# Kernel tuning notes

Hardware: AMD Instinct MI355X
Metric: run time of the kernel (lower is better)

The kernel has to match this reference:

```python
import jax, jax.numpy as jnp
import numpy as np

N = 50000
E = 800000
H = 128
K = 4
BN_EPS = 1e-5


def _cheb_norm(edge_index):
    # PyG ChebConv with normalization='sym', lambda_max=2.0:
    # L_hat = 2L/lambda_max - I = -D^{-1/2} A D^{-1/2}
    src, dst = edge_index[0], edge_index[1]
    deg = jax.ops.segment_sum(jnp.ones((E,), jnp.float32), src, num_segments=N)
    dinv = jnp.where(deg > 0, jax.lax.rsqrt(jnp.maximum(deg, 1.0)), 0.0)
    return -dinv[src] * dinv[dst]  # [E]


def _cheb_conv(x, src, dst, w, W, b):
    # Chebyshev recursion: Tx0=x, Tx1=L_hat x, Txk = 2 L_hat Tx_{k-1} - Tx_{k-2}
    def prop(h):
        return jax.ops.segment_sum(h[src] * w[:, None], dst, num_segments=N)
    Tx0 = x
    out = Tx0 @ W[0]
    Tx1 = prop(Tx0)
    out = out + Tx1 @ W[1]
    for k in range(2, W.shape[0]):
        Tx2 = 2.0 * prop(Tx1) - Tx0
        out = out + Tx2 @ W[k]
        Tx0, Tx1 = Tx1, Tx2
    return out + b


def _bn(h, gamma, beta):
    # BatchNorm1d, training mode: biased batch stats over nodes
    m = h.mean(axis=0)
    v = h.var(axis=0)
    return (h - m) * jax.lax.rsqrt(v + BN_EPS) * gamma + beta


def setup_inputs() -> dict:
    key = jax.random.key(0)
    ks = jax.random.split(key, 8)
    x = jax.random.normal(ks[0], (N, 3), jnp.float32)
    edge_index = jax.random.randint(ks[1], (2, E), 0, N, jnp.int64)
    s1 = 1.0 / np.sqrt(3)
    s2 = 1.0 / np.sqrt(H)
    d = {
        'x': x,
        'edge_index': edge_index,
        'W1': jax.random.normal(ks[2], (K, 3, H), jnp.float32) * s1,
        'b1': jnp.zeros((H,), jnp.float32),
        'W2': jax.random.normal(ks[3], (K, H, H), jnp.float32) * s2,
        'b2': jnp.zeros((H,), jnp.float32),
        'W3': jax.random.normal(ks[4], (K, H, H), jnp.float32) * s2,
        'b3': jnp.zeros((H,), jnp.float32),
        'W4': jax.random.normal(ks[5], (K, H, H), jnp.float32) * s2,
        'b4': jnp.zeros((H,), jnp.float32),
        'g1': jnp.ones((H,), jnp.float32), 'be1': jnp.zeros((H,), jnp.float32),
        'g2': jnp.ones((H,), jnp.float32), 'be2': jnp.zeros((H,), jnp.float32),
        'g3': jnp.ones((H,), jnp.float32), 'be3': jnp.zeros((H,), jnp.float32),
    }
    return d


def reference(x, edge_index, W1, b1, W2, b2, W3, b3, W4, b4, g1, be1, g2, be2, g3, be3):
    src, dst = edge_index[0], edge_index[1]
    w = _cheb_norm(edge_index)
    h = _bn(jax.nn.leaky_relu(_cheb_conv(x, src, dst, w, W1, b1)), g1, be1)
    h = _bn(jax.nn.leaky_relu(_cheb_conv(h, src, dst, w, W2, b2)), g2, be2)
    h = _bn(jax.nn.relu(_cheb_conv(h, src, dst, w, W3, b3)), g3, be3)
    h = _cheb_conv(h, src, dst, w, W4, b4)
    # F.normalize(p=2, dim=1)
    nrm = jnp.sqrt(jnp.sum(h * h, axis=1, keepdims=True))
    return h / jnp.maximum(nrm, 1e-12)
```

## Files before the change

kernel.cpp:

```cpp
#include <hip/hip_runtime.h>
#include <hip/hip_fp16.h>

#define NN 50000
#define NE 800000
#define HD 128
#define NSL 128
#define SLE (NE / NSL)
#define PW  12500

typedef __attribute__((ext_vector_type(8))) short short8;
typedef __attribute__((ext_vector_type(4))) float f32x4;
typedef __attribute__((ext_vector_type(4))) unsigned u32x4;

__device__ inline unsigned bf2pack(float lo, float hi) {
    unsigned a = __float_as_uint(lo); a = (a + 0x7fffu + ((a >> 16) & 1u)) >> 16;
    unsigned b = __float_as_uint(hi); b = (b + 0x7fffu + ((b >> 16) & 1u)) >> 16;
    return a | (b << 16);
}

__device__ inline float edgw(unsigned p) {
    return __half2float(__ushort_as_half((unsigned short)(p >> 16)));
}

__global__ __launch_bounds__(256) void k_hist(const int* __restrict__ ei,
                                              unsigned* __restrict__ phist) {
    __shared__ unsigned hist[PW];
    int b = blockIdx.x;
    int a = b >> 8;
    int s = (b & 255) >> 1;
    int c = b & 1;
    int tid = threadIdx.x;
    for (int i = tid; i < PW; i += 256) hist[i] = 0u;
    __syncthreads();
    const int* arr = ei + a * NE + s * SLE;
    int lo = c * 25000;
    for (int i = tid; i < SLE; i += 256) {
        int v = arr[i] - lo;
        if ((unsigned)v < 25000u)
            atomicAdd(&hist[v >> 1], 1u << ((v & 1) * 16));
    }
    __syncthreads();
    unsigned* dst = phist + (size_t)b * PW;
    for (int i = tid; i < PW; i += 256) dst[i] = hist[i];
}

__global__ __launch_bounds__(256) void k_hreduce(const unsigned* __restrict__ phist,
                                                 float* __restrict__ dinv,
                                                 int* __restrict__ cnt,
                                                 unsigned* __restrict__ pre) {
    int idx = blockIdx.x * 256 + threadIdx.x;
    if (idx >= 50000) return;
    int a = idx / 25000;
    int gw = idx % 25000;
    int c = gw / PW;
    int w = gw % PW;
    unsigned accLo = 0, accHi = 0;
    for (int s = 0; s < NSL; s++) {
        unsigned p = phist[(size_t)(((a * NSL + s) * 2 + c)) * PW + w];
        if (a == 1) pre[(size_t)s * 25000 + gw] = accLo | (accHi << 16);
        accLo += p & 0xffffu;
        accHi += p >> 16;
    }
    int b0 = c * 25000 + 2 * w;
    if (a == 0) {
        dinv[b0]     = accLo ? rsqrtf((float)accLo) : 0.0f;
        dinv[b0 + 1] = accHi ? rsqrtf((float)accHi) : 0.0f;
    } else {
        cnt[b0]     = (int)accLo;
        cnt[b0 + 1] = (int)accHi;
    }
}

__global__ __launch_bounds__(1024) void k_scan1(const int* __restrict__ cnt,
                                                int* __restrict__ rowptr,
                                                int* __restrict__ bsum) {
    __shared__ int s[1024];
    int tid = threadIdx.x;
    int gid = blockIdx.x * 1024 + tid;
    int v = (gid < NN) ? cnt[gid] : 0;
    s[tid] = v;
    __syncthreads();
    for (int off = 1; off < 1024; off <<= 1) {
        int t = 0;
        if (tid >= off) t = s[tid - off];
        __syncthreads();
        s[tid] += t;
        __syncthreads();
    }
    if (gid < NN) rowptr[gid] = s[tid] - v;
    if (tid == 1023) bsum[blockIdx.x] = s[1023];
}

__global__ void k_scan2(const int* __restrict__ bsum, int* __restrict__ boff,
                        int nb, int* __restrict__ rowptr) {
    if (threadIdx.x == 0 && blockIdx.x == 0) {
        int acc = 0;
        for (int i = 0; i < nb; i++) { boff[i] = acc; acc += bsum[i]; }
        rowptr[NN] = acc;
    }
}

__global__ void k_scan3(int* __restrict__ rowptr, const int* __restrict__ boff) {
    int i = blockIdx.x * 256 + threadIdx.x;
    if (i < NN) rowptr[i] += boff[i >> 10];
}

__global__ __launch_bounds__(256) void k_fill2(const int* __restrict__ ei,
                                               const float* __restrict__ dinv,
                                               const int* __restrict__ rowptr,
                                               const unsigned* __restrict__ pre,
                                               unsigned* __restrict__ edg) {
    __shared__ unsigned rank[PW];
    int b = blockIdx.x;
    int s = b >> 1;
    int c = b & 1;
    int tid = threadIdx.x;
    for (int i = tid; i < PW; i += 256) rank[i] = 0u;
    __syncthreads();
    int lo = c * 25000;
    const unsigned* preS = pre + (size_t)s * 25000 + c * PW;
    for (int i = tid; i < SLE; i += 256) {
        int e = s * SLE + i;
        int d = ei[NE + e];
        int v = d - lo;
        if ((unsigned)v < 25000u) {
            int src = ei[e];
            int w = v >> 1;
            int sh = (v & 1) * 16;
            unsigned r = atomicAdd(&rank[w], 1u << sh);
            r = (r >> sh) & 0xffffu;
            unsigned pw = (preS[w] >> sh) & 0xffffu;
            int pos = rowptr[d] + (int)pw + (int)r;
            unsigned short hw = __half_as_ushort(__float2half(-dinv[src] * dinv[d]));
            edg[pos] = (unsigned)src | ((unsigned)hw << 16);
        }
    }
}

__global__ void k_prop3(const float* __restrict__ h, const float* __restrict__ sub,
                        const int* __restrict__ rowptr, const unsigned* __restrict__ edg,
                        float* __restrict__ out) {
    int node = blockIdx.x * 256 + threadIdx.x;
    if (node >= NN) return;
    int e0 = rowptr[node], e1 = rowptr[node + 1];
    float a0 = 0.f, a1 = 0.f, a2 = 0.f;
    for (int e = e0; e < e1; e++) {
        unsigned p = edg[e];
        int s = p & 0xffffu;
        float v = edgw(p);
        a0 += v * h[s * 3 + 0];
        a1 += v * h[s * 3 + 1];
        a2 += v * h[s * 3 + 2];
    }
    if (sub) {
        a0 = 2.f * a0 - sub[node * 3 + 0];
        a1 = 2.f * a1 - sub[node * 3 + 1];
        a2 = 2.f * a2 - sub[node * 3 + 2];
    }
    out[node * 3 + 0] = a0;
    out[node * 3 + 1] = a1;
    out[node * 3 + 2] = a2;
}

#define ACC8(acc, u, v)                                               \
    acc[0] = fmaf(v, __uint_as_float(u[0] << 16), acc[0]);            \
    acc[1] = fmaf(v, __uint_as_float(u[0] & 0xffff0000u), acc[1]);    \
    acc[2] = fmaf(v, __uint_as_float(u[1] << 16), acc[2]);            \
    acc[3] = fmaf(v, __uint_as_float(u[1] & 0xffff0000u), acc[3]);    \
    acc[4] = fmaf(v, __uint_as_float(u[2] << 16), acc[4]);            \
    acc[5] = fmaf(v, __uint_as_float(u[2] & 0xffff0000u), acc[5]);    \
    acc[6] = fmaf(v, __uint_as_float(u[3] << 16), acc[6]);            \
    acc[7] = fmaf(v, __uint_as_float(u[3] & 0xffff0000u), acc[7]);

__global__ __launch_bounds__(256) void k_prop_pl(
        const unsigned short* __restrict__ h, const unsigned short* __restrict__ sub,
        const int* __restrict__ rowptr, const unsigned* __restrict__ edg,
        unsigned short* __restrict__ out) {
    int B = blockIdx.x;
    int xcd = B & 7;
    int c = xcd >> 1;
    int half = xcd & 1;
    int g = B >> 3;
    int n = (half * 392 + g) * 64 + (threadIdx.x >> 2);
    if (n >= NN) return;
    int lane4 = threadIdx.x & 3;
    int sl = lane4 * 8;
    int base = (threadIdx.x & 63) & ~3;
    const unsigned short* hp = h + (size_t)c * (NN * 32);
    int e0 = rowptr[n], e1 = rowptr[n + 1];
    float a[8] = {0, 0, 0, 0, 0, 0, 0, 0};
    float b[8] = {0, 0, 0, 0, 0, 0, 0, 0};
    int e = e0;
    for (; e + 8 <= e1; e += 8) {
        uint2 pp = *(const uint2*)(edg + e + lane4 * 2);
        unsigned q0 = __shfl(pp.x, base + 0, 64);
        unsigned q1 = __shfl(pp.y, base + 0, 64);
        unsigned q2 = __shfl(pp.x, base + 1, 64);
        unsigned q3 = __shfl(pp.y, base + 1, 64);
        unsigned q4 = __shfl(pp.x, base + 2, 64);
        unsigned q5 = __shfl(pp.y, base + 2, 64);
        unsigned q6 = __shfl(pp.x, base + 3, 64);
        unsigned q7 = __shfl(pp.y, base + 3, 64);
        u32x4 u0 = *(const u32x4*)(hp + (q0 & 0xffffu) * 32 + sl);
        u32x4 u1 = *(const u32x4*)(hp + (q1 & 0xffffu) * 32 + sl);
        u32x4 u2 = *(const u32x4*)(hp + (q2 & 0xffffu) * 32 + sl);
        u32x4 u3 = *(const u32x4*)(hp + (q3 & 0xffffu) * 32 + sl);
        u32x4 u4 = *(const u32x4*)(hp + (q4 & 0xffffu) * 32 + sl);
        u32x4 u5 = *(const u32x4*)(hp + (q5 & 0xffffu) * 32 + sl);
        u32x4 u6 = *(const u32x4*)(hp + (q6 & 0xffffu) * 32 + sl);
        u32x4 u7 = *(const u32x4*)(hp + (q7 & 0xffffu) * 32 + sl);
        float v0 = edgw(q0), v1 = edgw(q1), v2 = edgw(q2), v3 = edgw(q3);
        float v4 = edgw(q4), v5 = edgw(q5), v6 = edgw(q6), v7 = edgw(q7);
        ACC8(a, u0, v0)
        ACC8(b, u1, v1)
        ACC8(a, u2, v2)
        ACC8(b, u3, v3)
        ACC8(a, u4, v4)
        ACC8(b, u5, v5)
        ACC8(a, u6, v6)
        ACC8(b, u7, v7)
    }
    for (; e < e1; e++) {
        unsigned p = edg[e];
        u32x4 u = *(const u32x4*)(hp + (p & 0xffffu) * 32 + sl);
        float v = edgw(p);
        ACC8(a, u, v)
    }
    float r[8];
    #pragma unroll
    for (int q = 0; q < 8; q++) r[q] = a[q] + b[q];
    if (sub) {
        u32x4 su = __builtin_nontemporal_load(
            (const u32x4*)(sub + (size_t)c * (NN * 32) + n * 32 + sl));
        float s[8];
        s[0] = __uint_as_float(su[0] << 16); s[1] = __uint_as_float(su[0] & 0xffff0000u);
        s[2] = __uint_as_float(su[1] << 16); s[3] = __uint_as_float(su[1] & 0xffff0000u);
        s[4] = __uint_as_float(su[2] << 16); s[5] = __uint_as_float(su[2] & 0xffff0000u);
        s[6] = __uint_as_float(su[3] << 16); s[7] = __uint_as_float(su[3] & 0xffff0000u);
        #pragma unroll
        for (int q = 0; q < 8; q++) r[q] = 2.f * r[q] - s[q];
    }
    u32x4 o;
    o[0] = bf2pack(r[0], r[1]);
    o[1] = bf2pack(r[2], r[3]);
    o[2] = bf2pack(r[4], r[5]);
    o[3] = bf2pack(r[6], r[7]);
    __builtin_nontemporal_store(o, (u32x4*)(out + (size_t)c * (NN * 32) + n * 32 + sl));
}

__global__ void k_wconv_all(const float* __restrict__ W2, const float* __restrict__ W3,
                            const float* __restrict__ W4, unsigned short* __restrict__ Wb) {
    int gidx = blockIdx.x * 256 + threadIdx.x;
    int which = gidx >> 16;
    int idx = gidx & 65535;
    const float* W = which == 0 ? W2 : (which == 1 ? W3 : W4);
    int slot = idx >> 9;
    int lane = (idx >> 3) & 63;
    int j = idx & 7;
    int wg = slot >> 4;
    int t = slot & 15;
    int w = wg >> 1;
    int g = wg & 1;
    int k = t * 32 + (lane >> 4) * 8 + j;
    int col = w * 32 + g * 16 + (lane & 15);
    unsigned u = __float_as_uint(W[k * HD + col]);
    Wb[which * 65536 + idx] = (unsigned short)((u + 0x7fffu + ((u >> 16) & 1u)) >> 16);
}

__global__ __launch_bounds__(256) void k_gemmM(
        const unsigned short* __restrict__ A0, const unsigned short* __restrict__ A1,
        const unsigned short* __restrict__ A2, const unsigned short* __restrict__ A3,
        const unsigned short* __restrict__ Wb, const float* __restrict__ bias,
        float* __restrict__ outF, int act, float* __restrict__ gpart) {
    __shared__ unsigned short Asm[16 * 64 * 8];
    const int tid = threadIdx.x;
    const int w = tid >> 6;
    const int lane = tid & 63;
    const int l15 = lane & 15;
    const int quad = lane >> 4;

    short8 Bf[16][2];
    #pragma unroll
    for (int t = 0; t < 16; t++) {
        #pragma unroll
        for (int g = 0; g < 2; g++) {
            int slot = (w * 2 + g) * 16 + t;
            Bf[t][g] = *(const short8*)(Wb + slot * 512 + lane * 8);
        }
    }
    float bcol[2];
    bcol[0] = bias[w * 32 + l15];
    bcol[1] = bias[w * 32 + 16 + l15];

    const unsigned short* Ap[4] = {A0, A1, A2, A3};
    float bnP[2] = {0.f, 0.f}, bnQ[2] = {0.f, 0.f};

    for (int tile = blockIdx.x; tile < NN / 16; tile += gridDim.x) {
        int r0 = tile * 16;
        __syncthreads();
        #pragma unroll
        for (int i = 0; i < 4; i++) {
            int idx = i * 256 + tid;
            int s = idx >> 6;
            int ln = idx & 63;
            const unsigned short* src = Ap[s >> 2] + (size_t)(s & 3) * (NN * 32)
                                        + (r0 + (ln & 15)) * 32 + (ln >> 4) * 8;
            *(uint4*)&Asm[idx * 8] = *(const uint4*)src;
        }
        __syncthreads();
        f32x4 acc0 = {0.f, 0.f, 0.f, 0.f};
        f32x4 acc1 = {0.f, 0.f, 0.f, 0.f};
        #pragma unroll
        for (int s = 0; s < 16; s++) {
            short8 af = *(const short8*)&Asm[(s * 64 + lane) * 8];
            acc0 = __builtin_amdgcn_mfma_f32_16x16x32_bf16(af, Bf[s][0], acc0, 0, 0, 0);
            acc1 = __builtin_amdgcn_mfma_f32_16x16x32_bf16(af, Bf[s][1], acc1, 0, 0, 0);
        }
        #pragma unroll
        for (int reg = 0; reg < 4; reg++) {
            int row = r0 + quad * 4 + reg;
            float v0 = acc0[reg] + bcol[0];
            float v1 = acc1[reg] + bcol[1];
            if (act == 1) {
                v0 = v0 > 0.f ? v0 : 0.01f * v0;
                v1 = v1 > 0.f ? v1 : 0.01f * v1;
            } else if (act == 2) {
                v0 = v0 > 0.f ? v0 : 0.f;
                v1 = v1 > 0.f ? v1 : 0.f;
            }
            outF[row * HD + w * 32 + l15] = v0;
            outF[row * HD + w * 32 + 16 + l15] = v1;
            bnP[0] += v0; bnQ[0] += v0 * v0;
            bnP[1] += v1; bnQ[1] += v1 * v1;
        }
    }
    if (gpart) {
        #pragma unroll
        for (int g = 0; g < 2; g++) {
            float p = bnP[g], q = bnQ[g];
            p += __shfl_xor(p, 16); p += __shfl_xor(p, 32);
            q += __shfl_xor(q, 16); q += __shfl_xor(q, 32);
            if (quad == 0) {
                int col = w * 32 + g * 16 + l15;
                gpart[col * 512 + blockIdx.x] = p;
                gpart[(128 + col) * 512 + blockIdx.x] = q;
            }
        }
    }
}

__global__ __launch_bounds__(256) void k_gemm1(
        const float* __restrict__ T0, const float* __restrict__ T1,
        const float* __restrict__ T2, const float* __restrict__ T3,
        const float* __restrict__ W, const float* __restrict__ bias,
        float* __restrict__ out) {
    __shared__ float Ws[12 * 128];
    __shared__ float tx[2][12];
    int t = threadIdx.x;
    for (int i = t; i < 12 * 128; i += 256) Ws[i] = W[i];
    int idx = blockIdx.x * 256 + t;
    int node = idx >> 7;
    int f = idx & 127;
    int localn = t >> 7;
    const float* Ts[4] = {T0, T1, T2, T3};
    if (f < 12 && node < NN) {
        tx[localn][f] = Ts[f / 3][node * 3 + (f % 3)];
    }
    __syncthreads();
    if (node < NN) {
        float acc = bias[f];
        #pragma unroll
        for (int c = 0; c < 12; c++) acc = fmaf(tx[localn][c], Ws[c * 128 + f], acc);
        acc = acc > 0.f ? acc : 0.01f * acc;
        out[node * HD + f] = acc;
    }
}

__global__ __launch_bounds__(256) void k_bnstats2(const float* __restrict__ h,
                                                  float* __restrict__ gpart) {
    __shared__ float red[512];
    int b = blockIdx.x;
    int f = threadIdx.x & 127;
    int half = threadIdx.x >> 7;
    int r0 = b * 98 + half;
    int r1 = b * 98 + 98;
    if (r1 > NN) r1 = NN;
    float s = 0.f, q = 0.f;
    for (int r = r0; r < r1; r += 2) {
        float v = __builtin_nontemporal_load(h + r * HD + f);
        s += v;
        q += v * v;
    }
    red[threadIdx.x] = s;
    red[256 + threadIdx.x] = q;
    __syncthreads();
    if (threadIdx.x < 128) {
        gpart[f * 512 + b] = red[threadIdx.x] + red[threadIdx.x + 128];
        gpart[(128 + f) * 512 + b] = red[256 + threadIdx.x] + red[384 + threadIdx.x];
    }
}

__global__ __launch_bounds__(128) void k_bnredfin(const float* __restrict__ gpart,
                                                  const float* __restrict__ g,
                                                  const float* __restrict__ be,
                                                  float* __restrict__ ss) {
    __shared__ float sm[2];
    int f = blockIdx.x;
    int wave = threadIdx.x >> 6;
    int lane = threadIdx.x & 63;
    const float* src = gpart + (size_t)(f + wave * 128) * 512;
    float s = 0.f;
    #pragma unroll
    for (int i = 0; i < 8; i++) s += src[i * 64 + lane];
    #pragma unroll
    for (int off = 32; off > 0; off >>= 1) s += __shfl_xor(s, off);
    if (lane == 0) sm[wave] = s;
    __syncthreads();
    if (threadIdx.x == 0) {
        float mean = sm[0] * (1.0f / NN);
        float var = sm[1] * (1.0f / NN) - mean * mean;
        float sc = g[f] * rsqrtf(var + 1e-5f);
        ss[f] = sc;
        ss[128 + f] = be[f] - mean * sc;
    }
}

__global__ void k_bncvt_pl(const float* __restrict__ h, const float* __restrict__ ss,
                           unsigned short* __restrict__ out) {
    int idx = blockIdx.x * 256 + threadIdx.x;
    if (idx < NN * 16) {
        int n = idx >> 4;
        int p = (idx >> 2) & 3;
        int q = idx & 3;
        const float4* hf = (const float4*)h;
        float4 v0 = hf[n * 32 + p * 8 + q * 2];
        float4 v1 = hf[n * 32 + p * 8 + q * 2 + 1];
        const float4* s4 = (const float4*)ss;
        float4 c0 = s4[p * 8 + q * 2];
        float4 c1 = s4[p * 8 + q * 2 + 1];
        float4 d0 = s4[32 + p * 8 + q * 2];
        float4 d1 = s4[32 + p * 8 + q * 2 + 1];
        v0.x = fmaf(v0.x, c0.x, d0.x); v0.y = fmaf(v0.y, c0.y, d0.y);
        v0.z = fmaf(v0.z, c0.z, d0.z); v0.w = fmaf(v0.w, c0.w, d0.w);
        v1.x = fmaf(v1.x, c1.x, d1.x); v1.y = fmaf(v1.y, c1.y, d1.y);
        v1.z = fmaf(v1.z, c1.z, d1.z); v1.w = fmaf(v1.w, c1.w, d1.w);
        uint4 o;
        o.x = bf2pack(v0.x, v0.y);
        o.y = bf2pack(v0.z, v0.w);
        o.z = bf2pack(v1.x, v1.y);
        o.w = bf2pack(v1.z, v1.w);
        ((uint4*)out)[(size_t)p * (NN * 4) + n * 4 + q] = o;
    }
}

__global__ __launch_bounds__(256) void k_l2norm(const float* __restrict__ h,
                                                float* __restrict__ out) {
    int row = blockIdx.x * 4 + (threadIdx.x >> 6);
    int lane = threadIdx.x & 63;
    if (row >= NN) return;
    float2 v = *(const float2*)(h + row * HD + lane * 2);
    float s = v.x * v.x + v.y * v.y;
    #pragma unroll
    for (int off = 32; off > 0; off >>= 1) s += __shfl_xor(s, off);
    float scale = 1.f / fmaxf(sqrtf(s), 1e-12f);
    *(float2*)(out + row * HD + lane * 2) = make_float2(v.x * scale, v.y * scale);
}

extern "C" void kernel_launch(void* const* d_in, const int* in_sizes, int n_in,
                              void* d_out, int out_size, void* d_ws, size_t ws_size,
                              hipStream_t stream) {
    const float* x  = (const float*)d_in[0];
    const int*   ei = (const int*)d_in[1];
    const float* W1 = (const float*)d_in[2];
    const float* b1 = (const float*)d_in[3];
    const float* W2 = (const float*)d_in[4];
    const float* b2 = (const float*)d_in[5];
    const float* W3 = (const float*)d_in[6];
    const float* b3 = (const float*)d_in[7];
    const float* W4 = (const float*)d_in[8];
    const float* b4 = (const float*)d_in[9];
    const float* g1 = (const float*)d_in[10];
    const float* be1 = (const float*)d_in[11];
    const float* g2 = (const float*)d_in[12];
    const float* be2 = (const float*)d_in[13];
    const float* g3 = (const float*)d_in[14];
    const float* be3 = (const float*)d_in[15];
    float* outp = (float*)d_out;

    char* base = (char*)d_ws;
    size_t off = 0;
    auto alloc = [&](size_t bytes) -> void* {
        void* p = base + off;
        off += (bytes + 255) & ~(size_t)255;
        return p;
    };
    float* dinv  = (float*)alloc(NN * 4);
    int*   cnt   = (int*)  alloc(NN * 4);
    int*   rowptr= (int*)  alloc((NN + 1) * 4);
    int*   bsum  = (int*)  alloc(64 * 4);
    int*   boff  = (int*)  alloc(64 * 4);
    float* ss    = (float*)alloc(256 * 4);
    float* gpart = (float*)alloc(256 * 512 * 4);
    unsigned short* Wb = (unsigned short*)alloc(3 * 512 * 128 * 2);
    unsigned* edg = (unsigned*)alloc((size_t)NE * 4);
    float* T3a   = (float*)alloc(NN * 3 * 4);
    float* T3b   = (float*)alloc(NN * 3 * 4);
    float* T3c   = (float*)alloc(NN * 3 * 4);
    float* F0    = (float*)alloc((size_t)NN * HD * 4);
    unsigned short* Bb0 = (unsigned short*)alloc((size_t)NN * HD * 2);
    unsigned short* Bb1 = (unsigned short*)alloc((size_t)NN * HD * 2);
    unsigned short* Bb2 = (unsigned short*)alloc((size_t)NN * HD * 2);
    unsigned short* Bb3 = (unsigned short*)alloc((size_t)NN * HD * 2);

    unsigned* pre   = (unsigned*)F0;
    unsigned* phist = (unsigned*)Bb0;

    const int gN = (NN + 255) / 256;
    const int nb = (NN + 1023) / 1024;

    k_hist<<<512, 256, 0, stream>>>(ei, phist);
    k_hreduce<<<(50000 + 255) / 256, 256, 0, stream>>>(phist, dinv, cnt, pre);
    k_scan1<<<nb, 1024, 0, stream>>>(cnt, rowptr, bsum);
    k_scan2<<<1, 64, 0, stream>>>(bsum, boff, nb, rowptr);
    k_scan3<<<gN, 256, 0, stream>>>(rowptr, boff);
    k_fill2<<<256, 256, 0, stream>>>(ei, dinv, rowptr, pre, edg);
    k_wconv_all<<<768, 256, 0, stream>>>(W2, W3, W4, Wb);

    const int gPP = 8 * 392;
    const int gG = 512;
    const int gCvt = NN * 16 / 256;
    const int gL2 = (NN + 3) / 4;
    unsigned short* Wb2 = Wb;
    unsigned short* Wb3 = Wb + 65536;
    unsigned short* Wb4 = Wb + 131072;

    k_prop3<<<gN, 256, 0, stream>>>(x, nullptr, rowptr, edg, T3a);
    k_prop3<<<gN, 256, 0, stream>>>(T3a, x, rowptr, edg, T3b);
    k_prop3<<<gN, 256, 0, stream>>>(T3b, T3a, rowptr, edg, T3c);
    k_gemm1<<<(NN * 128 + 255) / 256, 256, 0, stream>>>(x, T3a, T3b, T3c, W1, b1, F0);
    k_bnstats2<<<512, 256, 0, stream>>>(F0, gpart);
    k_bnredfin<<<128, 128, 0, stream>>>(gpart, g1, be1, ss);
    k_bncvt_pl<<<gCvt, 256, 0, stream>>>(F0, ss, Bb0);

    k_prop_pl<<<gPP, 256, 0, stream>>>(Bb0, nullptr, rowptr, edg, Bb1);
    k_prop_pl<<<gPP, 256, 0, stream>>>(Bb1, Bb0, rowptr, edg, Bb2);
    k_prop_pl<<<gPP, 256, 0, stream>>>(Bb2, Bb1, rowptr, edg, Bb3);
    k_gemmM<<<gG, 256, 0, stream>>>(Bb0, Bb1, Bb2, Bb3, Wb2, b2, F0, 1, gpart);
    k_bnredfin<<<128, 128, 0, stream>>>(gpart, g2, be2, ss);
    k_bncvt_pl<<<gCvt, 256, 0, stream>>>(F0, ss, Bb0);

    k_prop_pl<<<gPP, 256, 0, stream>>>(Bb0, nullptr, rowptr, edg, Bb1);
    k_prop_pl<<<gPP, 256, 0, stream>>>(Bb1, Bb0, rowptr, edg, Bb2);
    k_prop_pl<<<gPP, 256, 0, stream>>>(Bb2, Bb1, rowptr, edg, Bb3);
    k_gemmM<<<gG, 256, 0, stream>>>(Bb0, Bb1, Bb2, Bb3, Wb3, b3, F0, 2, gpart);
    k_bnredfin<<<128, 128, 0, stream>>>(gpart, g3, be3, ss);
    k_bncvt_pl<<<gCvt, 256, 0, stream>>>(F0, ss, Bb0);

    k_prop_pl<<<gPP, 256, 0, stream>>>(Bb0, nullptr, rowptr, edg, Bb1);
    k_prop_pl<<<gPP, 256, 0, stream>>>(Bb1, Bb0, rowptr, edg, Bb2);
    k_prop_pl<<<gPP, 256, 0, stream>>>(Bb2, Bb1, rowptr, edg, Bb3);
    k_gemmM<<<gG, 256, 0, stream>>>(Bb0, Bb1, Bb2, Bb3, Wb4, b4, F0, 0, nullptr);
    k_l2norm<<<gL2, 256, 0, stream>>>(F0, outp);

    (void)n_in; (void)in_sizes; (void)out_size; (void)ws_size;
}
```

Measured before the change: 619.3 us.

## Fuse BN stats into gemm1, L2 norm into last GEMM, and tune prop tails

Several independent changes. The layer-1 dense step now also computes the BatchNorm partial sums, which removes a separate stats pass over F0. The final GEMM applies the row L2 normalisation itself through shuffles and shared memory, so the extra k_l2norm kernel and its F0 round trip go away. The prop kernels get a handled remainder path (a single shuffled 8-edge step and a padded edge buffer), an unrolled 3-channel prop with dual accumulators and a smaller block size, and a wave-shuffle block scan replacing the serial k_scan2.

Result: faster. 544.8 us (-12.0%).

```diff
diff --git a/kernel.cpp b/kernel.cpp
--- a/kernel.cpp
+++ b/kernel.cpp
@@ -93,11 +93,16 @@
 
 __global__ void k_scan2(const int* __restrict__ bsum, int* __restrict__ boff,
                         int nb, int* __restrict__ rowptr) {
-    if (threadIdx.x == 0 && blockIdx.x == 0) {
-        int acc = 0;
-        for (int i = 0; i < nb; i++) { boff[i] = acc; acc += bsum[i]; }
-        rowptr[NN] = acc;
-    }
+    int lane = threadIdx.x;
+    int v = (lane < nb) ? bsum[lane] : 0;
+    int s = v;
+    #pragma unroll
+    for (int off = 1; off < 64; off <<= 1) {
+        int t = __shfl_up(s, off, 64);
+        if (lane >= off) s += t;
+    }
+    if (lane < nb) boff[lane] = s - v;
+    if (lane == 63) rowptr[NN] = s;
 }
 
 __global__ void k_scan3(int* __restrict__ rowptr, const int* __restrict__ boff) {
@@ -137,21 +142,45 @@
     }
 }
 
-__global__ void k_prop3(const float* __restrict__ h, const float* __restrict__ sub,
+__global__ __launch_bounds__(128) void k_prop3(const float* __restrict__ h,
+                        const float* __restrict__ sub,
                         const int* __restrict__ rowptr, const unsigned* __restrict__ edg,
                         float* __restrict__ out) {
-    int node = blockIdx.x * 256 + threadIdx.x;
+    int node = blockIdx.x * 128 + threadIdx.x;
     if (node >= NN) return;
     int e0 = rowptr[node], e1 = rowptr[node + 1];
     float a0 = 0.f, a1 = 0.f, a2 = 0.f;
-    for (int e = e0; e < e1; e++) {
-        unsigned p = edg[e];
-        int s = p & 0xffffu;
-        float v = edgw(p);
-        a0 += v * h[s * 3 + 0];
-        a1 += v * h[s * 3 + 1];
-        a2 += v * h[s * 3 + 2];
-    }
+    float c0 = 0.f, c1 = 0.f, c2 = 0.f;
+    int e = e0;
+    for (; e + 4 <= e1; e += 4) {
+        unsigned p0 = edg[e], p1 = edg[e + 1], p2 = edg[e + 2], p3 = edg[e + 3];
+        int s0 = (int)(p0 & 0xffffu) * 3, s1 = (int)(p1 & 0xffffu) * 3;
+        int s2 = (int)(p2 & 0xffffu) * 3, s3 = (int)(p3 & 0xffffu) * 3;
+        float x0 = h[s0], y0 = h[s0 + 1], z0 = h[s0 + 2];
+        float x1 = h[s1], y1 = h[s1 + 1], z1 = h[s1 + 2];
+        float x2 = h[s2], y2 = h[s2 + 1], z2 = h[s2 + 2];
+        float x3 = h[s3], y3 = h[s3 + 1], z3 = h[s3 + 2];
+        float w0 = edgw(p0), w1 = edgw(p1), w2 = edgw(p2), w3 = edgw(p3);
+        a0 = fmaf(w0, x0, a0); a1 = fmaf(w0, y0, a1); a2 = fmaf(w0, z0, a2);
+        c0 = fmaf(w1, x1, c0); c1 = fmaf(w1, y1, c1); c2 = fmaf(w1, z1, c2);
+        a0 = fmaf(w2, x2, a0); a1 = fmaf(w2, y2, a1); a2 = fmaf(w2, z2, a2);
+        c0 = fmaf(w3, x3, c0); c1 = fmaf(w3, y3, c1); c2 = fmaf(w3, z3, c2);
+    }
+    if (e < e1) {
+        unsigned p0 = edg[e];
+        unsigned p1 = (e + 1 < e1) ? edg[e + 1] : 0u;
+        unsigned p2 = (e + 2 < e1) ? edg[e + 2] : 0u;
+        int s0 = (int)(p0 & 0xffffu) * 3, s1 = (int)(p1 & 0xffffu) * 3;
+        int s2 = (int)(p2 & 0xffffu) * 3;
+        float x0 = h[s0], y0 = h[s0 + 1], z0 = h[s0 + 2];
+        float x1 = h[s1], y1 = h[s1 + 1], z1 = h[s1 + 2];
+        float x2 = h[s2], y2 = h[s2 + 1], z2 = h[s2 + 2];
+        float w0 = edgw(p0), w1 = edgw(p1), w2 = edgw(p2);
+        a0 = fmaf(w0, x0, a0); a1 = fmaf(w0, y0, a1); a2 = fmaf(w0, z0, a2);
+        c0 = fmaf(w1, x1, c0); c1 = fmaf(w1, y1, c1); c2 = fmaf(w1, z1, c2);
+        a0 = fmaf(w2, x2, a0); a1 = fmaf(w2, y2, a1); a2 = fmaf(w2, z2, a2);
+    }
+    a0 += c0; a1 += c1; a2 += c2;
     if (sub) {
         a0 = 2.f * a0 - sub[node * 3 + 0];
         a1 = 2.f * a1 - sub[node * 3 + 1];
@@ -220,11 +249,42 @@
         ACC8(a, u6, v6)
         ACC8(b, u7, v7)
     }
-    for (; e < e1; e++) {
-        unsigned p = edg[e];
-        u32x4 u = *(const u32x4*)(hp + (p & 0xffffu) * 32 + sl);
-        float v = edgw(p);
-        ACC8(a, u, v)
+    int rem = e1 - e;
+    if (rem > 0) {
+        uint2 pp = *(const uint2*)(edg + e + lane4 * 2);
+        unsigned q0 = __shfl(pp.x, base + 0, 64);
+        unsigned q1 = __shfl(pp.y, base + 0, 64);
+        unsigned q2 = __shfl(pp.x, base + 1, 64);
+        unsigned q3 = __shfl(pp.y, base + 1, 64);
+        unsigned q4 = __shfl(pp.x, base + 2, 64);
+        unsigned q5 = __shfl(pp.y, base + 2, 64);
+        unsigned q6 = __shfl(pp.x, base + 3, 64);
+        unsigned q7 = __shfl(pp.y, base + 3, 64);
+        q1 = (rem > 1) ? q1 : 0u;
+        q2 = (rem > 2) ? q2 : 0u;
+        q3 = (rem > 3) ? q3 : 0u;
+        q4 = (rem > 4) ? q4 : 0u;
+        q5 = (rem > 5) ? q5 : 0u;
+        q6 = (rem > 6) ? q6 : 0u;
+        q7 = 0u;
+        u32x4 u0 = *(const u32x4*)(hp + (q0 & 0xffffu) * 32 + sl);
+        u32x4 u1 = *(const u32x4*)(hp + (q1 & 0xffffu) * 32 + sl);
+        u32x4 u2 = *(const u32x4*)(hp + (q2 & 0xffffu) * 32 + sl);
+        u32x4 u3 = *(const u32x4*)(hp + (q3 & 0xffffu) * 32 + sl);
+        u32x4 u4 = *(const u32x4*)(hp + (q4 & 0xffffu) * 32 + sl);
+        u32x4 u5 = *(const u32x4*)(hp + (q5 & 0xffffu) * 32 + sl);
+        u32x4 u6 = *(const u32x4*)(hp + (q6 & 0xffffu) * 32 + sl);
+        u32x4 u7 = *(const u32x4*)(hp + (q7 & 0xffffu) * 32 + sl);
+        float v0 = edgw(q0), v1 = edgw(q1), v2 = edgw(q2), v3 = edgw(q3);
+        float v4 = edgw(q4), v5 = edgw(q5), v6 = edgw(q6), v7 = edgw(q7);
+        ACC8(a, u0, v0)
+        ACC8(b, u1, v1)
+        ACC8(a, u2, v2)
+        ACC8(b, u3, v3)
+        ACC8(a, u4, v4)
+        ACC8(b, u5, v5)
+        ACC8(a, u6, v6)
+        ACC8(b, u7, v7)
     }
     float r[8];
     #pragma unroll
@@ -273,6 +333,7 @@
         const unsigned short* __restrict__ Wb, const float* __restrict__ bias,
         float* __restrict__ outF, int act, float* __restrict__ gpart) {
     __shared__ unsigned short Asm[16 * 64 * 8];
+    __shared__ float sred[64];
     const int tid = threadIdx.x;
     const int w = tid >> 6;
     const int lane = tid & 63;
@@ -316,22 +377,54 @@
             acc0 = __builtin_amdgcn_mfma_f32_16x16x32_bf16(af, Bf[s][0], acc0, 0, 0, 0);
             acc1 = __builtin_amdgcn_mfma_f32_16x16x32_bf16(af, Bf[s][1], acc1, 0, 0, 0);
         }
-        #pragma unroll
-        for (int reg = 0; reg < 4; reg++) {
-            int row = r0 + quad * 4 + reg;
-            float v0 = acc0[reg] + bcol[0];
-            float v1 = acc1[reg] + bcol[1];
-            if (act == 1) {
-                v0 = v0 > 0.f ? v0 : 0.01f * v0;
-                v1 = v1 > 0.f ? v1 : 0.01f * v1;
-            } else if (act == 2) {
-                v0 = v0 > 0.f ? v0 : 0.f;
-                v1 = v1 > 0.f ? v1 : 0.f;
+        if (act == 3) {
+            float vv0[4], vv1[4], rs[4];
+            #pragma unroll
+            for (int reg = 0; reg < 4; reg++) {
+                float v0 = acc0[reg] + bcol[0];
+                float v1 = acc1[reg] + bcol[1];
+                vv0[reg] = v0; vv1[reg] = v1;
+                float s2 = v0 * v0 + v1 * v1;
+                s2 += __shfl_xor(s2, 1);
+                s2 += __shfl_xor(s2, 2);
+                s2 += __shfl_xor(s2, 4);
+                s2 += __shfl_xor(s2, 8);
+                rs[reg] = s2;
             }
-            outF[row * HD + w * 32 + l15] = v0;
-            outF[row * HD + w * 32 + 16 + l15] = v1;
-            bnP[0] += v0; bnQ[0] += v0 * v0;
-            bnP[1] += v1; bnQ[1] += v1 * v1;
+            if (l15 == 0) {
+                #pragma unroll
+                for (int reg = 0; reg < 4; reg++)
+                    sred[w * 16 + quad * 4 + reg] = rs[reg];
+            }
+            __syncthreads();
+            #pragma unroll
+            for (int reg = 0; reg < 4; reg++) {
+                int row16 = quad * 4 + reg;
+                float tot = sred[row16] + sred[16 + row16]
+                          + sred[32 + row16] + sred[48 + row16];
+                float sc = 1.f / fmaxf(sqrtf(tot), 1e-12f);
+                int row = r0 + row16;
+                outF[row * HD + w * 32 + l15] = vv0[reg] * sc;
+                outF[row * HD + w * 32 + 16 + l15] = vv1[reg] * sc;
+            }
+        } else {
+            #pragma unroll
+            for (int reg = 0; reg < 4; reg++) {
+                int row = r0 + quad * 4 + reg;
+                float v0 = acc0[reg] + bcol[0];
+                float v1 = acc1[reg] + bcol[1];
+                if (act == 1) {
+                    v0 = v0 > 0.f ? v0 : 0.01f * v0;
+                    v1 = v1 > 0.f ? v1 : 0.01f * v1;
+                } else if (act == 2) {
+                    v0 = v0 > 0.f ? v0 : 0.f;
+                    v1 = v1 > 0.f ? v1 : 0.f;
+                }
+                outF[row * HD + w * 32 + l15] = v0;
+                outF[row * HD + w * 32 + 16 + l15] = v1;
+                bnP[0] += v0; bnQ[0] += v0 * v0;
+                bnP[1] += v1; bnQ[1] += v1 * v1;
+            }
         }
     }
     if (gpart) {
@@ -353,50 +446,38 @@
         const float* __restrict__ T0, const float* __restrict__ T1,
         const float* __restrict__ T2, const float* __restrict__ T3,
         const float* __restrict__ W, const float* __restrict__ bias,
-        float* __restrict__ out) {
+        float* __restrict__ out, float* __restrict__ gpart) {
     __shared__ float Ws[12 * 128];
-    __shared__ float tx[2][12];
+    __shared__ float red[512];
     int t = threadIdx.x;
     for (int i = t; i < 12 * 128; i += 256) Ws[i] = W[i];
-    int idx = blockIdx.x * 256 + t;
-    int node = idx >> 7;
-    int f = idx & 127;
-    int localn = t >> 7;
+    __syncthreads();
+    int f = t & 127;
+    int half = t >> 7;
+    float bs = bias[f];
+    float bP = 0.f, bQ = 0.f;
+    int r0 = blockIdx.x * 98;
+    int r1 = r0 + 98;
+    if (r1 > NN) r1 = NN;
     const float* Ts[4] = {T0, T1, T2, T3};
-    if (f < 12 && node < NN) {
-        tx[localn][f] = Ts[f / 3][node * 3 + (f % 3)];
-    }
+    for (int n = r0 + half; n < r1; n += 2) {
+        float acc = bs;
+        #pragma unroll
+        for (int c = 0; c < 12; c++) {
+            float tv = Ts[c / 3][n * 3 + (c % 3)];
+            acc = fmaf(tv, Ws[c * 128 + f], acc);
+        }
+        acc = acc > 0.f ? acc : 0.01f * acc;
+        out[n * HD + f] = acc;
+        bP += acc;
+        bQ += acc * acc;
+    }
+    red[t] = bP;
+    red[256 + t] = bQ;
     __syncthreads();
-    if (node < NN) {
-        float acc = bias[f];
-        #pragma unroll
-        for (int c = 0; c < 12; c++) acc = fmaf(tx[localn][c], Ws[c * 128 + f], acc);
-        acc = acc > 0.f ? acc : 0.01f * acc;
-        out[node * HD + f] = acc;
-    }
-}
-
-__global__ __launch_bounds__(256) void k_bnstats2(const float* __restrict__ h,
-                                                  float* __restrict__ gpart) {
-    __shared__ float red[512];
-    int b = blockIdx.x;
-    int f = threadIdx.x & 127;
-    int half = threadIdx.x >> 7;
-    int r0 = b * 98 + half;
-    int r1 = b * 98 + 98;
-    if (r1 > NN) r1 = NN;
-    float s = 0.f, q = 0.f;
-    for (int r = r0; r < r1; r += 2) {
-        float v = __builtin_nontemporal_load(h + r * HD + f);
-        s += v;
-        q += v * v;
-    }
-    red[threadIdx.x] = s;
-    red[256 + threadIdx.x] = q;
-    __syncthreads();
-    if (threadIdx.x < 128) {
-        gpart[f * 512 + b] = red[threadIdx.x] + red[threadIdx.x + 128];
-        gpart[(128 + f) * 512 + b] = red[256 + threadIdx.x] + red[384 + threadIdx.x];
+    if (t < 128) {
+        gpart[t * 512 + blockIdx.x] = red[t] + red[t + 128];
+        gpart[(128 + t) * 512 + blockIdx.x] = red[256 + t] + red[256 + t + 128];
     }
 }
 
@@ -453,19 +534,6 @@
     }
 }
 
-__global__ __launch_bounds__(256) void k_l2norm(const float* __restrict__ h,
-                                                float* __restrict__ out) {
-    int row = blockIdx.x * 4 + (threadIdx.x >> 6);
-    int lane = threadIdx.x & 63;
-    if (row >= NN) return;
-    float2 v = *(const float2*)(h + row * HD + lane * 2);
-    float s = v.x * v.x + v.y * v.y;
-    #pragma unroll
-    for (int off = 32; off > 0; off >>= 1) s += __shfl_xor(s, off);
-    float scale = 1.f / fmaxf(sqrtf(s), 1e-12f);
-    *(float2*)(out + row * HD + lane * 2) = make_float2(v.x * scale, v.y * scale);
-}
-
 extern "C" void kernel_launch(void* const* d_in, const int* in_sizes, int n_in,
                               void* d_out, int out_size, void* d_ws, size_t ws_size,
                               hipStream_t stream) {
@@ -502,7 +570,7 @@
     float* ss    = (float*)alloc(256 * 4);
     float* gpart = (float*)alloc(256 * 512 * 4);
     unsigned short* Wb = (unsigned short*)alloc(3 * 512 * 128 * 2);
-    unsigned* edg = (unsigned*)alloc((size_t)NE * 4);
+    unsigned* edg = (unsigned*)alloc((size_t)(NE + 8) * 4);
     float* T3a   = (float*)alloc(NN * 3 * 4);
     float* T3b   = (float*)alloc(NN * 3 * 4);
     float* T3c   = (float*)alloc(NN * 3 * 4);
@@ -516,6 +584,7 @@
     unsigned* phist = (unsigned*)Bb0;
 
     const int gN = (NN + 255) / 256;
+    const int gP3 = (NN + 127) / 128;
     const int nb = (NN + 1023) / 1024;
 
     k_hist<<<512, 256, 0, stream>>>(ei, phist);
@@ -529,16 +598,14 @@
     const int gPP = 8 * 392;
     const int gG = 512;
     const int gCvt = NN * 16 / 256;
-    const int gL2 = (NN + 3) / 4;
     unsigned short* Wb2 = Wb;
     unsigned short* Wb3 = Wb + 65536;
     unsigned short* Wb4 = Wb + 131072;
 
-    k_prop3<<<gN, 256, 0, stream>>>(x, nullptr, rowptr, edg, T3a);
-    k_prop3<<<gN, 256, 0, stream>>>(T3a, x, rowptr, edg, T3b);
-    k_prop3<<<gN, 256, 0, stream>>>(T3b, T3a, rowptr, edg, T3c);
-    k_gemm1<<<(NN * 128 + 255) / 256, 256, 0, stream>>>(x, T3a, T3b, T3c, W1, b1, F0);
-    k_bnstats2<<<512, 256, 0, stream>>>(F0, gpart);
+    k_prop3<<<gP3, 128, 0, stream>>>(x, nullptr, rowptr, edg, T3a);
+    k_prop3<<<gP3, 128, 0, stream>>>(T3a, x, rowptr, edg, T3b);
+    k_prop3<<<gP3, 128, 0, stream>>>(T3b, T3a, rowptr, edg, T3c);
+    k_gemm1<<<512, 256, 0, stream>>>(x, T3a, T3b, T3c, W1, b1, F0, gpart);
     k_bnredfin<<<128, 128, 0, stream>>>(gpart, g1, be1, ss);
     k_bncvt_pl<<<gCvt, 256, 0, stream>>>(F0, ss, Bb0);
 
@@ -559,8 +626,7 @@
     k_prop_pl<<<gPP, 256, 0, stream>>>(Bb0, nullptr, rowptr, edg, Bb1);
     k_prop_pl<<<gPP, 256, 0, stream>>>(Bb1, Bb0, rowptr, edg, Bb2);
     k_prop_pl<<<gPP, 256, 0, stream>>>(Bb2, Bb1, rowptr, edg, Bb3);
-    k_gemmM<<<gG, 256, 0, stream>>>(Bb0, Bb1, Bb2, Bb3, Wb4, b4, F0, 0, nullptr);
-    k_l2norm<<<gL2, 256, 0, stream>>>(F0, outp);
+    k_gemmM<<<gG, 256, 0, stream>>>(Bb0, Bb1, Bb2, Bb3, Wb4, b4, outp, 3, nullptr);
 
     (void)n_in; (void)in_sizes; (void)out_size; (void)ws_size;
 }
```
